# Kernel optimization log

Hardware: AMD Instinct MI355X
Metric: run time of the kernel (lower is better)

Reference implementation:

```python
import jax, jax.numpy as jnp
import numpy as np

EPS = 1e-5
NEG_SLOPE = 0.2
GN_GROUPS = 8


def conv2d(x, w, b):
    # x: [B,C,H,W], w: [O,I,3,3]
    y = jax.lax.conv_general_dilated(
        x, w, window_strides=(1, 1), padding=((1, 1), (1, 1)),
        dimension_numbers=('NCHW', 'OIHW', 'NCHW'))
    return y + b[None, :, None, None]


def conv3d_d(x, w, b):
    # x: [B,C,D,H,W], w: [O,I,3,1,1] -> conv along D only
    y = jax.lax.conv_general_dilated(
        x, w, window_strides=(1, 1, 1), padding=((1, 1), (0, 0), (0, 0)),
        dimension_numbers=('NCDHW', 'OIDHW', 'NCDHW'))
    return y + b[None, :, None, None, None]


def group_norm(x, gamma, beta):
    # x: [B,C,D,H,W]; normalize per group over (C/g, D, H, W)
    B, C, D, H, W = x.shape
    xg = x.reshape(B, GN_GROUPS, C // GN_GROUPS, D, H, W)
    mu = jnp.mean(xg, axis=(2, 3, 4, 5), keepdims=True)
    var = jnp.var(xg, axis=(2, 3, 4, 5), keepdims=True)
    xn = ((xg - mu) * jax.lax.rsqrt(var + EPS)).reshape(B, C, D, H, W)
    return xn * gamma[None, :, None, None, None] + beta[None, :, None, None, None]


def setup_inputs() -> dict:
    key = jax.random.key(0)
    ks = jax.random.split(key, 8)
    C = 32
    B, D, H, W = 2, 24, 160, 160
    s = lambda fan: 1.0 / np.sqrt(fan)
    return {
        'x': jax.random.normal(ks[0], (B, C, D, H, W), jnp.float32),
        'w_f1': jax.random.normal(ks[1], (2 * C, C, 3, 1, 1), jnp.float32) * s(C * 3),
        'b_f1': jnp.zeros((2 * C,), jnp.float32),
        'gn_g': jnp.ones((2 * C,), jnp.float32),
        'gn_b': jnp.zeros((2 * C,), jnp.float32),
        'w_f2': jax.random.normal(ks[2], (C, 2 * C, 3, 1, 1), jnp.float32) * s(2 * C * 3),
        'b_f2': jnp.zeros((C,), jnp.float32),
        'w_u': jax.random.normal(ks[3], (C, 2 * C, 3, 3), jnp.float32) * s(2 * C * 9),
        'b_u': jnp.zeros((C,), jnp.float32),
        'w_r': jax.random.normal(ks[4], (C, 2 * C, 3, 3), jnp.float32) * s(2 * C * 9),
        'b_r': jnp.zeros((C,), jnp.float32),
        'w_o': jax.random.normal(ks[5], (C, 2 * C, 3, 3), jnp.float32) * s(2 * C * 9),
        'b_o': jnp.zeros((C,), jnp.float32),
    }


def reference(x, w_f1, b_f1, gn_g, gn_b, w_f2, b_f2, w_u, b_u, w_r, b_r, w_o, b_o):
    B, C, D, H, W = x.shape

    # slice_flow: Conv3d(C->2C,(3,1,1)) -> GroupNorm(8) -> LeakyReLU(0.2) -> Conv3d(2C->C,(3,1,1))
    sf = conv3d_d(x, w_f1, b_f1)
    sf = group_norm(sf, gn_g, gn_b)
    sf = jnp.where(sf >= 0, sf, NEG_SLOPE * sf)
    slice_features = conv3d_d(sf, w_f2, b_f2)

    def gru_step(h, xd):
        combined = jnp.concatenate([xd, h], axis=1)
        update = jax.nn.sigmoid(conv2d(combined, w_u, b_u))
        reset = jax.nn.sigmoid(conv2d(combined, w_r, b_r))
        combined_reset = jnp.concatenate([xd, reset * h], axis=1)
        cand = jnp.tanh(conv2d(combined_reset, w_o, b_o))
        h_new = (1.0 - update) * h + update * cand
        return h_new, h_new

    xd = jnp.moveaxis(x, 2, 0)  # [D,B,C,H,W]
    h0 = jnp.zeros((B, C, H, W), x.dtype)
    _, fwd = jax.lax.scan(gru_step, h0, xd)                 # [D,B,C,H,W]
    _, bwd = jax.lax.scan(gru_step, h0, xd, reverse=True)   # aligned with xd order

    enhanced = xd + fwd + bwd                                # [D,B,C,H,W]
    return jnp.moveaxis(enhanced, 0, 2) + slice_features
```

## Files before the change

kernel.cpp:

```cpp
#include <hip/hip_runtime.h>
#include <hip/hip_bf16.h>
#include <stdint.h>

#define EPS_GN 1e-5f
#define NEG_SLOPE 0.2f

static constexpr int  Bn   = 2;
static constexpr int  Cn   = 32;
static constexpr int  Dn   = 24;
static constexpr int  Hn   = 160;
static constexpr int  Wn   = 160;
static constexpr int  HWn  = Hn * Wn;
static constexpr long DHWn = (long)Dn * HWn;
static constexpr long NPIX = (long)Bn * Dn * HWn;

using frag8  = __attribute__((ext_vector_type(8)))  short;
using accf16 = __attribute__((ext_vector_type(16))) float;

__device__ __forceinline__ float bf2f(__hip_bfloat16 v) { return __bfloat162float(v); }
__device__ __forceinline__ __hip_bfloat16 f2bf(float v) { return __float2bfloat16(v); }
__device__ __forceinline__ float sigm(float v) { return 1.f / (1.f + __expf(-v)); }
__device__ __forceinline__ float tanh_(float v) {
    float e = __expf(2.f * v);
    return 1.f - 2.f / (e + 1.f);
}

__global__ __launch_bounds__(256) void bpack1_kernel(
    const float* __restrict__ w, __hip_bfloat16* __restrict__ dst)
{
    int t = blockIdx.x * 256 + threadIdx.x;
    if (t >= 6 * 2 * 64 * 8) return;
    int j    = t & 7;
    int lane = (t >> 3) & 63;
    int idx  = t >> 9;
    int nt   = idx & 1;
    int kb   = idx >> 1;
    int o    = nt * 32 + (lane & 31);
    int k    = kb * 16 + (lane >> 5) * 8 + j;
    int ci   = k & 31;
    int kd   = k >> 5;
    dst[t] = f2bf(w[(o * 32 + ci) * 3 + kd]);
}

__global__ __launch_bounds__(256) void bpack2_kernel(
    const float* __restrict__ w, __hip_bfloat16* __restrict__ dst)
{
    int t = blockIdx.x * 256 + threadIdx.x;
    if (t >= 12 * 64 * 8) return;
    int j    = t & 7;
    int lane = (t >> 3) & 63;
    int kb   = t >> 9;
    int o    = lane & 31;
    int k    = kb * 16 + (lane >> 5) * 8 + j;
    int ci   = k & 63;
    int kd   = k >> 6;
    dst[t] = f2bf(w[(o * 64 + ci) * 3 + kd]);
}

__global__ __launch_bounds__(256) void bpack_kernel(
    const float* __restrict__ w, __hip_bfloat16* __restrict__ dst)
{
    int t = blockIdx.x * 256 + threadIdx.x;
    if (t >= 9 * 4 * 64 * 8) return;
    int j    = t & 7;
    int lane = (t >> 3) & 63;
    int kb   = (t >> 9) & 3;
    int tap  = t >> 11;
    int ci   = kb * 16 + (lane >> 5) * 8 + j;
    int o    = lane & 31;
    dst[t] = f2bf(w[(o * 64 + ci) * 9 + tap]);
}

__global__ __launch_bounds__(256) void tohwc_kernel(
    const float* __restrict__ x, __hip_bfloat16* __restrict__ xhwc)
{
    __shared__ float tile[32][65];
    int bd = blockIdx.y;
    int b  = bd / Dn, d = bd % Dn;
    int p0 = blockIdx.x * 64;
    const float* xb = x + (long)b * Cn * DHWn + (long)d * HWn + p0;
    for (int e = threadIdx.x; e < 2048; e += 256) {
        int c = e >> 6, p = e & 63;
        tile[c][p] = xb[(long)c * DHWn + p];
    }
    __syncthreads();
    __hip_bfloat16* ob = xhwc + ((long)bd * HWn + p0) * 32;
    for (int e = threadIdx.x; e < 2048; e += 256) {
        int p = e >> 5, c = e & 31;
        ob[p * 32 + c] = f2bf(tile[c][p]);
    }
}

__global__ __launch_bounds__(256) void conv1_mfma(
    const __hip_bfloat16* __restrict__ xhwc,
    const __hip_bfloat16* __restrict__ Bp1,
    const float* __restrict__ b1,
    int b,
    __hip_bfloat16* __restrict__ A,
    float* __restrict__ gsum, float* __restrict__ gsq)
{
    int wave = threadIdx.x >> 6;
    int lane = threadIdx.x & 63;
    int ml   = lane & 31;
    int kh   = lane >> 5;
    int tile0 = blockIdx.x * 8 + wave * 2;

    frag8 bf[6][2];
#pragma unroll
    for (int kb = 0; kb < 6; kb++)
#pragma unroll
        for (int nt = 0; nt < 2; nt++)
            bf[kb][nt] = *(const frag8*)(Bp1 + ((kb * 2 + nt) * 64 + lane) * 8);

    int d  = tile0 / 800;
    int p0 = (tile0 % 800) * 32;

    accf16 acc[2][2];
#pragma unroll
    for (int t = 0; t < 2; t++)
#pragma unroll
        for (int nt = 0; nt < 2; nt++)
#pragma unroll
            for (int i = 0; i < 16; i++) acc[t][nt][i] = 0.f;

    for (int kd = 0; kd < 3; kd++) {
        int dd = d + kd - 1;
        bool valid = (unsigned)dd < (unsigned)Dn;
        const __hip_bfloat16* rp = xhwc + ((long)(b * Dn + dd) * HWn) * 32;
#pragma unroll
        for (int h2 = 0; h2 < 2; h2++) {
            int kb = kd * 2 + h2;
#pragma unroll
            for (int t = 0; t < 2; t++) {
                frag8 a = {};
                if (valid)
                    a = *(const frag8*)(rp + (long)(p0 + t * 32 + ml) * 32 + h2 * 16 + kh * 8);
                acc[t][0] = __builtin_amdgcn_mfma_f32_32x32x16_bf16(a, bf[kb][0], acc[t][0], 0, 0, 0);
                acc[t][1] = __builtin_amdgcn_mfma_f32_32x32x16_bf16(a, bf[kb][1], acc[t][1], 0, 0, 0);
            }
        }
    }

    float bias[2] = { b1[ml], b1[32 + ml] };
    float s[2] = {0.f, 0.f}, q[2] = {0.f, 0.f};
    __hip_bfloat16* Ap = A + (long)d * HWn * 64;
#pragma unroll
    for (int t = 0; t < 2; t++) {
        int pb = p0 + t * 32;
#pragma unroll
        for (int nt = 0; nt < 2; nt++) {
#pragma unroll
            for (int i = 0; i < 16; i++) {
                int row = (i & 3) + 8 * (i >> 2) + 4 * kh;
                float v = acc[t][nt][i] + bias[nt];
                Ap[(long)(pb + row) * 64 + nt * 32 + ml] = f2bf(v);
                s[nt] += v;
                q[nt] += v * v;
            }
        }
    }
#pragma unroll
    for (int nt = 0; nt < 2; nt++) {
        s[nt] += __shfl_xor(s[nt], 32);
        q[nt] += __shfl_xor(q[nt], 32);
    }
    __shared__ float ss[64], sq[64];
    if (threadIdx.x < 64) { ss[threadIdx.x] = 0.f; sq[threadIdx.x] = 0.f; }
    __syncthreads();
    if (lane < 32) {
        atomicAdd(&ss[ml],      s[0]); atomicAdd(&sq[ml],      q[0]);
        atomicAdd(&ss[32 + ml], s[1]); atomicAdd(&sq[32 + ml], q[1]);
    }
    __syncthreads();
    if (threadIdx.x < 64) {
        atomicAdd(&gsum[b * 64 + threadIdx.x], ss[threadIdx.x]);
        atomicAdd(&gsq [b * 64 + threadIdx.x], sq[threadIdx.x]);
    }
}

__global__ __launch_bounds__(64) void finalize_kernel(
    const float* __restrict__ gsum, const float* __restrict__ gsq,
    const float* __restrict__ gn_g, const float* __restrict__ gn_b,
    float* __restrict__ scal, float* __restrict__ shft, int b)
{
    int ci = threadIdx.x;
    if (ci >= 64) return;
    int g = ci >> 3;
    float s = 0.f, qq = 0.f;
#pragma unroll
    for (int k = 0; k < 8; k++) {
        s  += gsum[b * 64 + g * 8 + k];
        qq += gsq [b * 64 + g * 8 + k];
    }
    float N   = 8.0f * (float)DHWn;
    float mu  = s / N;
    float var = qq / N - mu * mu;
    float rs  = rsqrtf(var + EPS_GN);
    float scv = rs * gn_g[ci];
    scal[b * 64 + ci] = scv;
    shft[b * 64 + ci] = gn_b[ci] - mu * scv;
}

__global__ __launch_bounds__(256) void act_kernel(
    __hip_bfloat16* __restrict__ A,
    const float* __restrict__ scal, const float* __restrict__ shft, int b)
{
    __shared__ float sc[64], sh[64];
    if (threadIdx.x < 64) {
        sc[threadIdx.x] = scal[b * 64 + threadIdx.x];
        sh[threadIdx.x] = shft[b * 64 + threadIdx.x];
    }
    __syncthreads();
    long i0 = ((long)blockIdx.x * 256 + threadIdx.x) * 8;
    __hip_bfloat16 loc[8];
    *(frag8*)loc = *(const frag8*)(A + i0);
    int c0 = (int)(i0 & 63);
#pragma unroll
    for (int j = 0; j < 8; j++) {
        float f  = bf2f(loc[j]);
        float an = fmaf(f, sc[c0 + j], sh[c0 + j]);
        loc[j]   = f2bf(fmaxf(an, NEG_SLOPE * an));
    }
    *(frag8*)(A + i0) = *(frag8*)loc;
}

__global__ __launch_bounds__(256) void conv2_mfma(
    const __hip_bfloat16* __restrict__ Aact,
    const __hip_bfloat16* __restrict__ Bp2,
    const float* __restrict__ b2,
    const float* __restrict__ x,
    float* __restrict__ out,
    int b)
{
    int wave = threadIdx.x >> 6;
    int lane = threadIdx.x & 63;
    int ml   = lane & 31;
    int kh   = lane >> 5;
    int tile = blockIdx.x * 4 + wave;

    frag8 bf[12];
#pragma unroll
    for (int kb = 0; kb < 12; kb++)
        bf[kb] = *(const frag8*)(Bp2 + (kb * 64 + lane) * 8);

    int d  = tile / 800;
    int p0 = (tile % 800) * 32;

    accf16 acc;
#pragma unroll
    for (int i = 0; i < 16; i++) acc[i] = 0.f;

    for (int kd = 0; kd < 3; kd++) {
        int dd = d + kd - 1;
        bool valid = (unsigned)dd < (unsigned)Dn;
        const __hip_bfloat16* rp = Aact + (long)dd * HWn * 64;
#pragma unroll
        for (int qq = 0; qq < 4; qq++) {
            frag8 a = {};
            if (valid)
                a = *(const frag8*)(rp + (long)(p0 + ml) * 64 + qq * 16 + kh * 8);
            acc = __builtin_amdgcn_mfma_f32_32x32x16_bf16(a, bf[kd * 4 + qq], acc, 0, 0, 0);
        }
    }

    __shared__ float tb[4][32][33];
    float bias = b2[ml];
    const float* xb = x   + (long)b * Cn * DHWn + (long)d * HWn;
    float*       ob = out + (long)b * Cn * DHWn + (long)d * HWn;
#pragma unroll
    for (int i = 0; i < 16; i++) {
        int row = (i & 3) + 8 * (i >> 2) + 4 * kh;
        tb[wave][row][ml] = acc[i] + bias;
    }
#pragma unroll
    for (int r2 = 0; r2 < 16; r2++) {
        int c = r2 * 2 + kh;
        float v = tb[wave][ml][c] + xb[(long)c * DHWn + p0 + ml];
        ob[(long)c * DHWn + p0 + ml] = v;
    }
}

__global__ __launch_bounds__(256) void gru_r_mfma(
    const __hip_bfloat16* __restrict__ xhwc,
    int dfwd, int dbwd,
    const __hip_bfloat16* __restrict__ hold,
    const __hip_bfloat16* __restrict__ Br,
    const float* __restrict__ br,
    __hip_bfloat16* __restrict__ rhbf)
{
    int db   = blockIdx.y;
    int dir  = db >> 1, b = db & 1;
    int d    = dir ? dbwd : dfwd;
    int wave = threadIdx.x >> 6;
    int lane = threadIdx.x & 63;
    int ml   = lane & 31;
    int kh   = lane >> 5;

    const __hip_bfloat16* xb = xhwc + ((long)b * Dn + d) * HWn * 32;
    const __hip_bfloat16* hb = hold + (long)db * HWn * 32;

    int tile = blockIdx.x * 4 + wave;
    int pb   = tile * 32;
    int py0  = pb / Wn, px0 = pb % Wn;

    accf16 ar;
#pragma unroll
    for (int i = 0; i < 16; i++) ar[i] = 0.f;

    for (int tap = 0; tap < 9; tap++) {
        int dy = tap / 3 - 1, dx = tap % 3 - 1;
        int yy = py0 + dy;
        int xx = px0 + ml + dx;
        bool ok  = ((unsigned)yy < (unsigned)Hn) & ((unsigned)xx < (unsigned)Wn);
        long poff = ((long)(yy * Wn + xx)) * 32;
#pragma unroll
        for (int kb = 0; kb < 4; kb++) {
            frag8 brf = *(const frag8*)(Br + ((tap * 4 + kb) * 64 + lane) * 8);
            int ch = kb * 16 + kh * 8;
            const __hip_bfloat16* bsel = (kb < 2) ? (xb + ch) : (hb + (ch - 32));
            frag8 a = {};
            if (ok) a = *(const frag8*)(bsel + poff);
            ar = __builtin_amdgcn_mfma_f32_32x32x16_bf16(a, brf, ar, 0, 0, 0);
        }
    }

    float bias_r = br[ml];
    __hip_bfloat16* rhb = rhbf + (long)db * HWn * 32;
#pragma unroll
    for (int i = 0; i < 16; i++) {
        int row = (i & 3) + 8 * (i >> 2) + 4 * kh;
        int pix = pb + row;
        float hp = bf2f(hb[(long)pix * 32 + ml]);
        float rr = sigm(ar[i] + bias_r);
        rhb[(long)pix * 32 + ml] = f2bf(rr * hp);
    }
}

__global__ __launch_bounds__(256) void gru_cand_mfma(
    const __hip_bfloat16* __restrict__ xhwc,
    int dfwd, int dbwd,
    const __hip_bfloat16* __restrict__ hold,
    const __hip_bfloat16* __restrict__ rhbf,
    const __hip_bfloat16* __restrict__ Bu,
    const __hip_bfloat16* __restrict__ Bo,
    const float* __restrict__ bu, const float* __restrict__ bo,
    __hip_bfloat16* __restrict__ hnew,
    float* __restrict__ out)
{
    int db   = blockIdx.y;
    int dir  = db >> 1, b = db & 1;
    int d    = dir ? dbwd : dfwd;
    int wave = threadIdx.x >> 6;
    int lane = threadIdx.x & 63;
    int ml   = lane & 31;
    int kh   = lane >> 5;

    const __hip_bfloat16* xb  = xhwc + ((long)b * Dn + d) * HWn * 32;
    const __hip_bfloat16* hb  = hold + (long)db * HWn * 32;
    const __hip_bfloat16* rhb = rhbf + (long)db * HWn * 32;
    __hip_bfloat16*       hnb = hnew + (long)db * HWn * 32;

    int tile = blockIdx.x * 4 + wave;
    int pb   = tile * 32;
    int py0  = pb / Wn, px0 = pb % Wn;

    accf16 au, ao;
#pragma unroll
    for (int i = 0; i < 16; i++) { au[i] = 0.f; ao[i] = 0.f; }

    for (int tap = 0; tap < 9; tap++) {
        int dy = tap / 3 - 1, dx = tap % 3 - 1;
        int yy = py0 + dy;
        int xx = px0 + ml + dx;
        bool ok  = ((unsigned)yy < (unsigned)Hn) & ((unsigned)xx < (unsigned)Wn);
        long poff = ((long)(yy * Wn + xx)) * 32;
#pragma unroll
        for (int kb = 0; kb < 4; kb++) {
            frag8 buf = *(const frag8*)(Bu + ((tap * 4 + kb) * 64 + lane) * 8);
            frag8 bof = *(const frag8*)(Bo + ((tap * 4 + kb) * 64 + lane) * 8);
            int ch = kb * 16 + kh * 8;
            if (kb < 2) {
                frag8 a = {};
                if (ok) a = *(const frag8*)(xb + ch + poff);
                au = __builtin_amdgcn_mfma_f32_32x32x16_bf16(a, buf, au, 0, 0, 0);
                ao = __builtin_amdgcn_mfma_f32_32x32x16_bf16(a, bof, ao, 0, 0, 0);
            } else {
                frag8 ah = {}, arh = {};
                if (ok) {
                    ah  = *(const frag8*)(hb  + (ch - 32) + poff);
                    arh = *(const frag8*)(rhb + (ch - 32) + poff);
                }
                au = __builtin_amdgcn_mfma_f32_32x32x16_bf16(ah,  buf, au, 0, 0, 0);
                ao = __builtin_amdgcn_mfma_f32_32x32x16_bf16(arh, bof, ao, 0, 0, 0);
            }
        }
    }

    __shared__ float tb[4][32][33];
    float bias_u = bu[ml], bias_o = bo[ml];
    float* ob = out + (long)b * Cn * DHWn + (long)d * HWn;
#pragma unroll
    for (int i = 0; i < 16; i++) {
        int row = (i & 3) + 8 * (i >> 2) + 4 * kh;
        int pix = pb + row;
        float uu = sigm(au[i] + bias_u);
        float cc = tanh_(ao[i] + bias_o);
        float hp = bf2f(hb[(long)pix * 32 + ml]);
        float hn = (1.f - uu) * hp + uu * cc;
        hnb[(long)pix * 32 + ml] = f2bf(hn);
        tb[wave][row][ml] = hn;
    }
#pragma unroll
    for (int r2 = 0; r2 < 16; r2++) {
        int c = r2 * 2 + kh;
        ob[(long)c * DHWn + pb + ml] += tb[wave][ml][c];
    }
}

extern "C" void kernel_launch(void* const* d_in, const int* in_sizes, int n_in,
                              void* d_out, int out_size, void* d_ws, size_t ws_size,
                              hipStream_t stream)
{
    const float* x    = (const float*)d_in[0];
    const float* w_f1 = (const float*)d_in[1];
    const float* b_f1 = (const float*)d_in[2];
    const float* gn_g = (const float*)d_in[3];
    const float* gn_b = (const float*)d_in[4];
    const float* w_f2 = (const float*)d_in[5];
    const float* b_f2 = (const float*)d_in[6];
    const float* w_u  = (const float*)d_in[7];
    const float* b_u  = (const float*)d_in[8];
    const float* w_r  = (const float*)d_in[9];
    const float* b_r  = (const float*)d_in[10];
    const float* w_o  = (const float*)d_in[11];
    const float* b_o  = (const float*)d_in[12];
    float* out = (float*)d_out;

    char* ws = (char*)d_ws;
    __hip_bfloat16* Bp1 = (__hip_bfloat16*)ws;
    __hip_bfloat16* Bp2 = Bp1 + 6144;
    __hip_bfloat16* Bu  = Bp2 + 6144;
    __hip_bfloat16* Br  = Bu + 18432;
    __hip_bfloat16* Bo  = Br + 18432;
    float* gsum = (float*)(Bo + 18432);
    float* gsq  = gsum + 128;
    float* scal = gsq + 128;
    float* shft = scal + 128;
    char* big = (char*)(shft + 128);
    big = (char*)(((uintptr_t)big + 255) & ~(uintptr_t)255);

    __hip_bfloat16* xhwc = (__hip_bfloat16*)big;
    __hip_bfloat16* Apre = (__hip_bfloat16*)(big + 78643200L);
    __hip_bfloat16* hA   = (__hip_bfloat16*)(big + 78643200L);
    __hip_bfloat16* hB   = (__hip_bfloat16*)(big + 85196800L);
    __hip_bfloat16* rhbf = (__hip_bfloat16*)(big + 91750400L);

    size_t need = (size_t)(big - ws) + 157286400UL;
    if (ws_size < need) return;

    bpack1_kernel<<<24, 256, 0, stream>>>(w_f1, Bp1);
    bpack2_kernel<<<24, 256, 0, stream>>>(w_f2, Bp2);
    bpack_kernel<<<72, 256, 0, stream>>>(w_u, Bu);
    bpack_kernel<<<72, 256, 0, stream>>>(w_r, Br);
    bpack_kernel<<<72, 256, 0, stream>>>(w_o, Bo);
    hipMemsetAsync(gsum, 0, 256 * sizeof(float), stream);

    tohwc_kernel<<<dim3(400, Bn * Dn), 256, 0, stream>>>(x, xhwc);

    for (int b = 0; b < Bn; b++) {
        conv1_mfma<<<2400, 256, 0, stream>>>(xhwc, Bp1, b_f1, b, Apre, gsum, gsq);
        finalize_kernel<<<1, 64, 0, stream>>>(gsum, gsq, gn_g, gn_b, scal, shft, b);
        act_kernel<<<19200, 256, 0, stream>>>(Apre, scal, shft, b);
        conv2_mfma<<<4800, 256, 0, stream>>>(Apre, Bp2, b_f2, x, out, b);
    }

    hipMemsetAsync(hA, 0, 6553600, stream);
    __hip_bfloat16* hbufs[2] = { hA, hB };
    for (int s = 0; s < Dn; s++) {
        int dfwd = s, dbwd = Dn - 1 - s;
        __hip_bfloat16* hold = hbufs[s & 1];
        __hip_bfloat16* hnew = hbufs[(s + 1) & 1];
        gru_r_mfma<<<dim3(200, 4), 256, 0, stream>>>(
            xhwc, dfwd, dbwd, hold, Br, b_r, rhbf);
        gru_cand_mfma<<<dim3(200, 4), 256, 0, stream>>>(
            xhwc, dfwd, dbwd, hold, rhbf, Bu, Bo, b_u, b_o, hnew, out);
    }
}
```

Before: 1.996 ms.

## Fuse GRU reset and candidate kernels using per-wave 2D tiles with halo recompute

After: 2.017 ms. No clear change (+1.0%).

```diff
diff --git a/kernel.cpp b/kernel.cpp
--- a/kernel.cpp
+++ b/kernel.cpp
@@ -103,7 +103,9 @@
     int lane = threadIdx.x & 63;
     int ml   = lane & 31;
     int kh   = lane >> 5;
-    int tile0 = blockIdx.x * 8 + wave * 2;
+    int bid  = blockIdx.x;
+    int sw   = (bid & 7) * 300 + (bid >> 3);
+    int tile0 = sw * 8 + wave * 2;
 
     frag8 bf[6][2];
 #pragma unroll
@@ -236,7 +238,9 @@
     int lane = threadIdx.x & 63;
     int ml   = lane & 31;
     int kh   = lane >> 5;
-    int tile = blockIdx.x * 4 + wave;
+    int bid  = blockIdx.x;
+    int sw   = (bid & 7) * 600 + (bid >> 3);
+    int tile = sw * 4 + wave;
 
     frag8 bf[12];
 #pragma unroll
@@ -280,13 +284,17 @@
     }
 }
 
-__global__ __launch_bounds__(256) void gru_r_mfma(
+__global__ __launch_bounds__(256) void gru_step_mfma(
     const __hip_bfloat16* __restrict__ xhwc,
     int dfwd, int dbwd,
     const __hip_bfloat16* __restrict__ hold,
+    const __hip_bfloat16* __restrict__ Bu,
     const __hip_bfloat16* __restrict__ Br,
-    const float* __restrict__ br,
-    __hip_bfloat16* __restrict__ rhbf)
+    const __hip_bfloat16* __restrict__ Bo,
+    const float* __restrict__ bu, const float* __restrict__ br,
+    const float* __restrict__ bo,
+    __hip_bfloat16* __restrict__ hnew,
+    float* __restrict__ out)
 {
     int db   = blockIdx.y;
     int dir  = db >> 1, b = db & 1;
@@ -296,124 +304,125 @@
     int ml   = lane & 31;
     int kh   = lane >> 5;
 
-    const __hip_bfloat16* xb = xhwc + ((long)b * Dn + d) * HWn * 32;
-    const __hip_bfloat16* hb = hold + (long)db * HWn * 32;
-
-    int tile = blockIdx.x * 4 + wave;
-    int pb   = tile * 32;
-    int py0  = pb / Wn, px0 = pb % Wn;
-
-    accf16 ar;
-#pragma unroll
-    for (int i = 0; i < 16; i++) ar[i] = 0.f;
-
-    for (int tap = 0; tap < 9; tap++) {
-        int dy = tap / 3 - 1, dx = tap % 3 - 1;
-        int yy = py0 + dy;
-        int xx = px0 + ml + dx;
-        bool ok  = ((unsigned)yy < (unsigned)Hn) & ((unsigned)xx < (unsigned)Wn);
-        long poff = ((long)(yy * Wn + xx)) * 32;
-#pragma unroll
-        for (int kb = 0; kb < 4; kb++) {
-            frag8 brf = *(const frag8*)(Br + ((tap * 4 + kb) * 64 + lane) * 8);
-            int ch = kb * 16 + kh * 8;
-            const __hip_bfloat16* bsel = (kb < 2) ? (xb + ch) : (hb + (ch - 32));
-            frag8 a = {};
-            if (ok) a = *(const frag8*)(bsel + poff);
-            ar = __builtin_amdgcn_mfma_f32_32x32x16_bf16(a, brf, ar, 0, 0, 0);
-        }
-    }
-
-    float bias_r = br[ml];
-    __hip_bfloat16* rhb = rhbf + (long)db * HWn * 32;
-#pragma unroll
-    for (int i = 0; i < 16; i++) {
-        int row = (i & 3) + 8 * (i >> 2) + 4 * kh;
-        int pix = pb + row;
-        float hp = bf2f(hb[(long)pix * 32 + ml]);
-        float rr = sigm(ar[i] + bias_r);
-        rhb[(long)pix * 32 + ml] = f2bf(rr * hp);
-    }
-}
-
-__global__ __launch_bounds__(256) void gru_cand_mfma(
-    const __hip_bfloat16* __restrict__ xhwc,
-    int dfwd, int dbwd,
-    const __hip_bfloat16* __restrict__ hold,
-    const __hip_bfloat16* __restrict__ rhbf,
-    const __hip_bfloat16* __restrict__ Bu,
-    const __hip_bfloat16* __restrict__ Bo,
-    const float* __restrict__ bu, const float* __restrict__ bo,
-    __hip_bfloat16* __restrict__ hnew,
-    float* __restrict__ out)
-{
-    int db   = blockIdx.y;
-    int dir  = db >> 1, b = db & 1;
-    int d    = dir ? dbwd : dfwd;
-    int wave = threadIdx.x >> 6;
-    int lane = threadIdx.x & 63;
-    int ml   = lane & 31;
-    int kh   = lane >> 5;
+    int bidx = blockIdx.x;
+    int sw   = (bidx & 7) * 25 + (bidx >> 3);
+    int tile = sw * 4 + wave;
+    int trow = tile / 20, tcol = tile % 20;
+    int py0  = trow * 4,  px0  = tcol * 8;
+
+    __shared__ __hip_bfloat16 rhl[4][64][40];
+    __shared__ float tb[4][32][33];
 
     const __hip_bfloat16* xb  = xhwc + ((long)b * Dn + d) * HWn * 32;
     const __hip_bfloat16* hb  = hold + (long)db * HWn * 32;
-    const __hip_bfloat16* rhb = rhbf + (long)db * HWn * 32;
     __hip_bfloat16*       hnb = hnew + (long)db * HWn * 32;
 
-    int tile = blockIdx.x * 4 + wave;
-    int pb   = tile * 32;
-    int py0  = pb / Wn, px0 = pb % Wn;
-
-    accf16 au, ao;
-#pragma unroll
-    for (int i = 0; i < 16; i++) { au[i] = 0.f; ao[i] = 0.f; }
-
-    for (int tap = 0; tap < 9; tap++) {
-        int dy = tap / 3 - 1, dx = tap % 3 - 1;
-        int yy = py0 + dy;
-        int xx = px0 + ml + dx;
-        bool ok  = ((unsigned)yy < (unsigned)Hn) & ((unsigned)xx < (unsigned)Wn);
-        long poff = ((long)(yy * Wn + xx)) * 32;
-#pragma unroll
-        for (int kb = 0; kb < 4; kb++) {
-            frag8 buf = *(const frag8*)(Bu + ((tap * 4 + kb) * 64 + lane) * 8);
-            frag8 bof = *(const frag8*)(Bo + ((tap * 4 + kb) * 64 + lane) * 8);
-            int ch = kb * 16 + kh * 8;
-            if (kb < 2) {
-                frag8 a = {};
-                if (ok) a = *(const frag8*)(xb + ch + poff);
-                au = __builtin_amdgcn_mfma_f32_32x32x16_bf16(a, buf, au, 0, 0, 0);
-                ao = __builtin_amdgcn_mfma_f32_32x32x16_bf16(a, bof, ao, 0, 0, 0);
-            } else {
-                frag8 ah = {}, arh = {};
-                if (ok) {
-                    ah  = *(const frag8*)(hb  + (ch - 32) + poff);
-                    arh = *(const frag8*)(rhb + (ch - 32) + poff);
+    float bias_r = br[ml], bias_u = bu[ml], bias_o = bo[ml];
+
+    {
+        int hr0 = ml / 10,        hc0 = ml - hr0 * 10;
+        int hp1 = 32 + ml;
+        int hr1 = hp1 / 10,       hc1 = hp1 - hr1 * 10;
+        int hy[2] = { py0 - 1 + hr0, py0 - 1 + hr1 };
+        int hx[2] = { px0 - 1 + hc0, px0 - 1 + hc1 };
+
+        accf16 ar[2];
+#pragma unroll
+        for (int t = 0; t < 2; t++)
+#pragma unroll
+            for (int i = 0; i < 16; i++) ar[t][i] = 0.f;
+
+        for (int tap = 0; tap < 9; tap++) {
+            int dy = tap / 3 - 1, dx = tap % 3 - 1;
+            bool ok[2]; long poff[2];
+#pragma unroll
+            for (int t = 0; t < 2; t++) {
+                int yy = hy[t] + dy, xx = hx[t] + dx;
+                ok[t]   = ((unsigned)yy < (unsigned)Hn) & ((unsigned)xx < (unsigned)Wn);
+                poff[t] = ((long)(yy * Wn + xx)) * 32;
+            }
+#pragma unroll
+            for (int kb = 0; kb < 4; kb++) {
+                frag8 brf = *(const frag8*)(Br + ((tap * 4 + kb) * 64 + lane) * 8);
+                int ch = kb * 16 + kh * 8;
+                const __hip_bfloat16* bsel = (kb < 2) ? (xb + ch) : (hb + (ch - 32));
+#pragma unroll
+                for (int t = 0; t < 2; t++) {
+                    frag8 a = {};
+                    if (ok[t]) a = *(const frag8*)(bsel + poff[t]);
+                    ar[t] = __builtin_amdgcn_mfma_f32_32x32x16_bf16(a, brf, ar[t], 0, 0, 0);
                 }
-                au = __builtin_amdgcn_mfma_f32_32x32x16_bf16(ah,  buf, au, 0, 0, 0);
-                ao = __builtin_amdgcn_mfma_f32_32x32x16_bf16(arh, bof, ao, 0, 0, 0);
-            }
-        }
-    }
-
-    __shared__ float tb[4][32][33];
-    float bias_u = bu[ml], bias_o = bo[ml];
-    float* ob = out + (long)b * Cn * DHWn + (long)d * HWn;
-#pragma unroll
-    for (int i = 0; i < 16; i++) {
-        int row = (i & 3) + 8 * (i >> 2) + 4 * kh;
-        int pix = pb + row;
-        float uu = sigm(au[i] + bias_u);
-        float cc = tanh_(ao[i] + bias_o);
-        float hp = bf2f(hb[(long)pix * 32 + ml]);
-        float hn = (1.f - uu) * hp + uu * cc;
-        hnb[(long)pix * 32 + ml] = f2bf(hn);
-        tb[wave][row][ml] = hn;
-    }
-#pragma unroll
-    for (int r2 = 0; r2 < 16; r2++) {
-        int c = r2 * 2 + kh;
-        ob[(long)c * DHWn + pb + ml] += tb[wave][ml][c];
+            }
+        }
+#pragma unroll
+        for (int t = 0; t < 2; t++) {
+#pragma unroll
+            for (int i = 0; i < 16; i++) {
+                int row = (i & 3) + 8 * (i >> 2) + 4 * kh;
+                int hp2 = t * 32 + row;
+                int hr  = hp2 / 10, hc = hp2 - hr * 10;
+                int hy2 = py0 - 1 + hr, hx2 = px0 - 1 + hc;
+                bool v  = ((unsigned)hy2 < (unsigned)Hn) & ((unsigned)hx2 < (unsigned)Wn);
+                float hpv = v ? bf2f(hb[((long)(hy2 * Wn + hx2)) * 32 + ml]) : 0.f;
+                rhl[wave][hp2][ml] = f2bf(sigm(ar[t][i] + bias_r) * hpv);
+            }
+        }
+    }
+
+    {
+        int prow = ml >> 3, pcol = ml & 7;
+        int oy = py0 + prow, ox = px0 + pcol;
+
+        accf16 au, ao;
+#pragma unroll
+        for (int i = 0; i < 16; i++) { au[i] = 0.f; ao[i] = 0.f; }
+
+        for (int tap = 0; tap < 9; tap++) {
+            int dy = tap / 3 - 1, dx = tap % 3 - 1;
+            int yy = oy + dy, xx = ox + dx;
+            bool ok  = ((unsigned)yy < (unsigned)Hn) & ((unsigned)xx < (unsigned)Wn);
+            long poff = ((long)(yy * Wn + xx)) * 32;
+            int hp = (prow + 1 + dy) * 10 + (pcol + 1 + dx);
+#pragma unroll
+            for (int kb = 0; kb < 4; kb++) {
+                frag8 buf = *(const frag8*)(Bu + ((tap * 4 + kb) * 64 + lane) * 8);
+                frag8 bof = *(const frag8*)(Bo + ((tap * 4 + kb) * 64 + lane) * 8);
+                int ch = kb * 16 + kh * 8;
+                if (kb < 2) {
+                    frag8 a = {};
+                    if (ok) a = *(const frag8*)(xb + ch + poff);
+                    au = __builtin_amdgcn_mfma_f32_32x32x16_bf16(a, buf, au, 0, 0, 0);
+                    ao = __builtin_amdgcn_mfma_f32_32x32x16_bf16(a, bof, ao, 0, 0, 0);
+                } else {
+                    frag8 ah = {};
+                    if (ok) ah = *(const frag8*)(hb + (ch - 32) + poff);
+                    au = __builtin_amdgcn_mfma_f32_32x32x16_bf16(ah, buf, au, 0, 0, 0);
+                    frag8 arh = *(const frag8*)(&rhl[wave][hp][(kb - 2) * 16 + kh * 8]);
+                    ao = __builtin_amdgcn_mfma_f32_32x32x16_bf16(arh, bof, ao, 0, 0, 0);
+                }
+            }
+        }
+
+        float* ob = out + (long)b * Cn * DHWn + (long)d * HWn;
+#pragma unroll
+        for (int i = 0; i < 16; i++) {
+            int lp  = (i & 3) + 8 * (i >> 2) + 4 * kh;
+            int pyy = py0 + (lp >> 3), pxx = px0 + (lp & 7);
+            long pix = (long)pyy * Wn + pxx;
+            float uu  = sigm(au[i] + bias_u);
+            float cc  = tanh_(ao[i] + bias_o);
+            float hpv = bf2f(hb[pix * 32 + ml]);
+            float hn  = (1.f - uu) * hpv + uu * cc;
+            hnb[pix * 32 + ml] = f2bf(hn);
+            tb[wave][lp][ml] = hn;
+        }
+        int pyy = py0 + (ml >> 3), pxx = px0 + (ml & 7);
+        long pix = (long)pyy * Wn + pxx;
+#pragma unroll
+        for (int r2 = 0; r2 < 16; r2++) {
+            int c = r2 * 2 + kh;
+            ob[(long)c * DHWn + pix] += tb[wave][ml][c];
+        }
     }
 }
 
@@ -453,7 +462,6 @@
     __hip_bfloat16* Apre = (__hip_bfloat16*)(big + 78643200L);
     __hip_bfloat16* hA   = (__hip_bfloat16*)(big + 78643200L);
     __hip_bfloat16* hB   = (__hip_bfloat16*)(big + 85196800L);
-    __hip_bfloat16* rhbf = (__hip_bfloat16*)(big + 91750400L);
 
     size_t need = (size_t)(big - ws) + 157286400UL;
     if (ws_size < need) return;
@@ -480,9 +488,7 @@
         int dfwd = s, dbwd = Dn - 1 - s;
         __hip_bfloat16* hold = hbufs[s & 1];
         __hip_bfloat16* hnew = hbufs[(s + 1) & 1];
-        gru_r_mfma<<<dim3(200, 4), 256, 0, stream>>>(
-            xhwc, dfwd, dbwd, hold, Br, b_r, rhbf);
-        gru_cand_mfma<<<dim3(200, 4), 256, 0, stream>>>(
-            xhwc, dfwd, dbwd, hold, rhbf, Bu, Bo, b_u, b_o, hnew, out);
-    }
-}
+        gru_step_mfma<<<dim3(200, 4), 256, 0, stream>>>(
+            xhwc, dfwd, dbwd, hold, Bu, Br, Bo, b_u, b_r, b_o, hnew, out);
+    }
+}
```
